# Performance work log

Hardware: AMD Instinct MI355X
Metric: run time of the kernel (lower is better)

The kernel has to match this reference:

```python
import jax, jax.numpy as jnp
import numpy as np

N_NODES = 50000
N_EDGES = 400000
NFEAT, NHID2, NHID3, NHID4, NCLASS = 500, 128, 128, 64, 40


def setup_inputs() -> dict:
    key = jax.random.key(0)
    ks = jax.random.split(key, 20)
    s = 0.05
    inp = {
        'x': jax.random.normal(ks[0], (N_NODES, NFEAT), jnp.float32),
        'src': jax.random.randint(ks[1], (4, N_EDGES), 0, N_NODES, jnp.int64 if jax.config.jax_enable_x64 else jnp.int32),
        'dst': jax.random.randint(ks[2], (4, N_EDGES), 0, N_NODES, jnp.int64 if jax.config.jax_enable_x64 else jnp.int32),
        'val': jax.random.uniform(ks[3], (4, N_EDGES), jnp.float32),
        'Wa': jax.random.normal(ks[4], (4, NFEAT, NHID2), jnp.float32) * s,
        'ba': jax.random.normal(ks[5], (4, NHID2), jnp.float32) * s,
        'Wb': jax.random.normal(ks[6], (4, NHID2, NHID3), jnp.float32) * s,
        'bb': jax.random.normal(ks[7], (4, NHID3), jnp.float32) * s,
        'Wc': jax.random.normal(ks[8], (4, NHID3, NHID4), jnp.float32) * s,
        'bc': jax.random.normal(ks[9], (4, NHID4), jnp.float32) * s,
        'dW': jax.random.normal(ks[10], (5, NHID4, NCLASS), jnp.float32) * s,
        'db': jax.random.normal(ks[11], (5, NCLASS), jnp.float32) * s,
        'e1W': jax.random.normal(ks[12], (4 * NHID4, NHID2), jnp.float32) * s,
        'e1b': jax.random.normal(ks[13], (NHID2,), jnp.float32) * s,
        'e2W': jax.random.normal(ks[14], (NHID2, NHID3), jnp.float32) * s,
        'e2b': jax.random.normal(ks[15], (NHID3,), jnp.float32) * s,
        'e3W': jax.random.normal(ks[16], (NHID3, NHID4), jnp.float32) * s,
        'e3b': jax.random.normal(ks[17], (NHID4,), jnp.float32) * s,
    }
    return inp


def _gcn(h, W, b, src, dst, val):
    # support = h @ W ; out = spmm(adj, support) + b  (Kipf GraphConvolution)
    support = h @ W                                   # [N, out]
    msg = support[src] * val[:, None]                 # [E, out] gather + scale
    return jax.ops.segment_sum(msg, dst, num_segments=N_NODES) + b


def reference(x, src, dst, val, Wa, ba, Wb, bb, Wc, bc, dW, db, e1W, e1b, e2W, e2b, e3W, e3b):
    # One GCN branch: relu(gcn) -> relu(gcn) -> gcn (dropout is inference no-op)
    def branch(Wa_i, ba_i, Wb_i, bb_i, Wc_i, bc_i, src_i, dst_i, val_i):
        h = jax.nn.relu(_gcn(x, Wa_i, ba_i, src_i, dst_i, val_i))
        h = jax.nn.relu(_gcn(h, Wb_i, bb_i, src_i, dst_i, val_i))
        return _gcn(h, Wc_i, bc_i, src_i, dst_i, val_i)  # pre-ReLU branch output

    xb = jax.vmap(branch)(Wa, ba, Wb, bb, Wc, bc, src, dst, val)  # [4, N, nhid4]

    # per-branch dense heads on relu(branch output)
    dense_out = jnp.einsum('knd,kdc->knc', jax.nn.relu(xb), dW[:4]) + db[:4, None, :]

    # ensemble MLP on concat(x1,x2,x3,x4)
    cat = jnp.transpose(xb, (1, 0, 2)).reshape(N_NODES, 4 * NHID4)
    e = jax.nn.relu(cat @ e1W + e1b)
    e = jax.nn.relu(e @ e2W + e2b)
    e = jax.nn.relu(e @ e3W + e3b)
    out5 = e @ dW[4] + db[4]

    return (dense_out[0], dense_out[1], dense_out[2], dense_out[3], out5)
```

## Files before the change

### kernel.cpp

```cpp
#include <hip/hip_runtime.h>
#include <stdint.h>

#define NN 50000
#define NE 400000
#define MPAD 50048
#define NF 500
#define KP 512
#define NBK 196

typedef __bf16 bf16;
typedef __bf16 bf16x8 __attribute__((ext_vector_type(8)));
typedef float  f32x4  __attribute__((ext_vector_type(4)));

__device__ __forceinline__ void gload16(const void* g, void* l) {
  __builtin_amdgcn_global_load_lds(
      (__attribute__((address_space(1))) void*)g,
      (__attribute__((address_space(3))) void*)l, 16, 0, 0);
}

__device__ __forceinline__ uint32_t packbf2(float a, float b) {
  union { bf16 h[2]; uint32_t u; } c;
  c.h[0] = (bf16)a; c.h[1] = (bf16)b;
  return c.u;
}

__global__ void k_conv_x(const float* __restrict__ x, bf16* __restrict__ xbf) {
  int idx = blockIdx.x * 256 + threadIdx.x;
  if (idx >= NN * KP) return;
  int n = idx >> 9, c = idx & (KP - 1);
  float v = (c < NF) ? x[n * NF + c] : 0.f;
  xbf[idx] = (bf16)v;
}

__global__ void k_conv_waT(const float* __restrict__ Wa, bf16* __restrict__ WaT) {
  int idx = blockIdx.x * 256 + threadIdx.x;
  if (idx >= 4 * 128 * KP) return;
  int b = idx >> 16;
  int r = idx & 65535;
  int n = r >> 9, k = r & 511;
  float v = (k < NF) ? Wa[(b * NF + k) * 128 + n] : 0.f;
  WaT[idx] = (bf16)v;
}

__global__ void k_conv_wT(const float* __restrict__ W, bf16* __restrict__ WT, int Kd, int Nd) {
  int idx = blockIdx.x * 256 + threadIdx.x;
  int tot = Kd * Nd;
  if (idx >= tot) return;
  int n = idx / Kd, k = idx - n * Kd;
  WT[(size_t)blockIdx.y * tot + idx] = (bf16)W[(size_t)blockIdx.y * tot + k * Nd + n];
}

__global__ void __launch_bounds__(256) k_bhist(const int* __restrict__ dst, int* __restrict__ bcnt) {
  __shared__ int h[256];
  int t = threadIdx.x;
  int z = blockIdx.z;
  h[t] = 0;
  __syncthreads();
  int e0 = blockIdx.x * 4096;
#pragma unroll
  for (int i = 0; i < 16; ++i) {
    int e = e0 + i * 256 + t;
    if (e < NE) atomicAdd(&h[dst[z * NE + e] >> 8], 1);
  }
  __syncthreads();
  if (t < NBK && h[t] > 0) atomicAdd(&bcnt[z * NBK + t], h[t]);
}

__global__ void __launch_bounds__(256) k_bscan(const int* __restrict__ bcnt,
                                               int* __restrict__ bases, int* __restrict__ gfill,
                                               int* __restrict__ offs) {
  __shared__ int ps[256];
  int t = threadIdx.x;
  for (int z = 0; z < 4; ++z) {
    int c = (t < NBK) ? bcnt[z * NBK + t] : 0;
    ps[t] = c;
    __syncthreads();
    for (int d = 1; d < 256; d <<= 1) {
      int v = (t >= d) ? ps[t - d] : 0;
      __syncthreads();
      ps[t] += v;
      __syncthreads();
    }
    if (t < NBK) {
      int ex = ps[t] - c;
      bases[z * (NBK + 1) + t] = ex;
      gfill[z * NBK + t] = ex;
      if (t == NBK - 1) bases[z * (NBK + 1) + NBK] = ps[t];
    }
    if (t == 0) offs[z * (NN + 1) + NN] = NE;
    __syncthreads();
  }
}

__global__ void __launch_bounds__(256) k_bin(const int* __restrict__ src, const int* __restrict__ dst,
                                             const float* __restrict__ val, int* __restrict__ gfill,
                                             int4* __restrict__ staging) {
  __shared__ int h[256];
  __shared__ int f2[256];
  __shared__ int base[256];
  int t = threadIdx.x;
  int z = blockIdx.z;
  h[t] = 0; f2[t] = 0;
  __syncthreads();
  int e0 = blockIdx.x * 4096;
  int se[16], sd[16], sv[16];
#pragma unroll
  for (int i = 0; i < 16; ++i) {
    int e = e0 + i * 256 + t;
    sd[i] = -1;
    if (e < NE) {
      sd[i] = dst[z * NE + e];
      se[i] = src[z * NE + e];
      sv[i] = ((const int*)val)[z * NE + e];
      atomicAdd(&h[sd[i] >> 8], 1);
    }
  }
  __syncthreads();
  if (t < NBK) {
    int c = h[t];
    base[t] = c ? atomicAdd(&gfill[z * NBK + t], c) : 0;
  }
  __syncthreads();
#pragma unroll
  for (int i = 0; i < 16; ++i) {
    if (sd[i] >= 0) {
      int bkt = sd[i] >> 8;
      int loc = atomicAdd(&f2[bkt], 1);
      staging[(size_t)z * NE + base[bkt] + loc] = make_int4(se[i], sd[i], sv[i], 0);
    }
  }
}

__global__ void __launch_bounds__(256) k_fine(const int4* __restrict__ staging,
                                              const int* __restrict__ bases,
                                              int* __restrict__ offs, int2* __restrict__ edata) {
  __shared__ int cnts[256];
  __shared__ int ps[256];
  __shared__ int exl[256];
  __shared__ int fl[256];
  int t = threadIdx.x;
  int z = blockIdx.z;
  int bkt = blockIdx.x;
  int base = bases[z * (NBK + 1) + bkt];
  int endp = bases[z * (NBK + 1) + bkt + 1];
  cnts[t] = 0; fl[t] = 0;
  __syncthreads();
  for (int e = base + t; e < endp; e += 256) {
    int dl = staging[(size_t)z * NE + e].y & 255;
    atomicAdd(&cnts[dl], 1);
  }
  __syncthreads();
  ps[t] = cnts[t];
  __syncthreads();
  for (int d = 1; d < 256; d <<= 1) {
    int v = (t >= d) ? ps[t - d] : 0;
    __syncthreads();
    ps[t] += v;
    __syncthreads();
  }
  exl[t] = ps[t] - cnts[t];
  int node0 = bkt * 256;
  if (node0 + t < NN) offs[z * (NN + 1) + node0 + t] = base + exl[t];
  __syncthreads();
  for (int e = base + t; e < endp; e += 256) {
    int4 g = staging[(size_t)z * NE + e];
    int dl = g.y & 255;
    int r = atomicAdd(&fl[dl], 1);
    edata[(size_t)z * NE + base + exl[dl] + r] = make_int2(g.x, g.z);
  }
}

template <int DIM>
__global__ void __launch_bounds__(256) k_spmm(
    const bf16* __restrict__ sup, const int* __restrict__ offs,
    const int2* __restrict__ edata,
    const float* __restrict__ bias, bf16* __restrict__ out,
    int ldOut, long long outBr, int relu) {
  constexpr int LPS = DIM / 8;
  constexpr int SLOTS = 64 / LPS;
  int b = blockIdx.z;
  int lane = threadIdx.x & 63;
  int slot = lane / LPS;
  int fl = lane % LPS;
  int n = blockIdx.x * 4 + (threadIdx.x >> 6);
  if (n >= NN) return;
  const int* o = offs + b * (NN + 1);
  int e0 = o[n], e1 = o[n + 1];
  const bf16* supb = sup + (size_t)b * MPAD * DIM;
  const int2* eb = edata + (size_t)b * NE;

  float a[8];
#pragma unroll
  for (int j = 0; j < 8; ++j) a[j] = 0.f;

  int e = e0 + slot;
  for (; e + SLOTS < e1; e += 2 * SLOTS) {
    int2 p0 = eb[e];
    int2 p1 = eb[e + SLOTS];
    float v0 = __int_as_float(p0.y);
    float v1 = __int_as_float(p1.y);
    bf16x8 r0 = *(const bf16x8*)(supb + (size_t)p0.x * DIM + fl * 8);
    bf16x8 r1 = *(const bf16x8*)(supb + (size_t)p1.x * DIM + fl * 8);
#pragma unroll
    for (int j = 0; j < 8; ++j) a[j] = fmaf(v0, (float)r0[j], a[j]);
#pragma unroll
    for (int j = 0; j < 8; ++j) a[j] = fmaf(v1, (float)r1[j], a[j]);
  }
  if (e < e1) {
    int2 p0 = eb[e];
    float v0 = __int_as_float(p0.y);
    bf16x8 r0 = *(const bf16x8*)(supb + (size_t)p0.x * DIM + fl * 8);
#pragma unroll
    for (int j = 0; j < 8; ++j) a[j] = fmaf(v0, (float)r0[j], a[j]);
  }

#pragma unroll
  for (int m = LPS; m < 64; m <<= 1) {
#pragma unroll
    for (int j = 0; j < 8; ++j) a[j] += __shfl_xor(a[j], m, 64);
  }

  if (slot == 0) {
    const float* bi = bias + b * DIM + fl * 8;
#pragma unroll
    for (int j = 0; j < 8; ++j) {
      a[j] += bi[j];
      if (relu) a[j] = fmaxf(a[j], 0.f);
    }
    union { bf16 h[8]; uint4 u4; } pk;
#pragma unroll
    for (int j = 0; j < 8; ++j) pk.h[j] = (bf16)a[j];
    *(uint4*)(out + (size_t)b * outBr + (size_t)n * ldOut + fl * 8) = pk.u4;
  }
}

template <int BN, bool BR>
__global__ void __launch_bounds__(256) k_gemm(
    const bf16* __restrict__ A, const bf16* __restrict__ B, bf16* __restrict__ C,
    const float* __restrict__ bias, int K, int ldA, int ldC,
    size_t sA, size_t sB, size_t sC) {
  constexpr int WN = BN / 2;
  constexpr int NFR = WN / 16;
  constexpr int BL = BN / 32;
  __shared__ __align__(16) unsigned char sa[128 * 128];
  __shared__ __align__(16) unsigned char sb[BN * 128];
  int tid = threadIdx.x;
  int lane = tid & 63;
  int wid = tid >> 6;
  int wm = wid & 1, wn = wid >> 1;
  const bf16* Ab = A + sA * blockIdx.z;
  const bf16* Bb = B + sB * blockIdx.z;
  bf16* Cb = C + sC * blockIdx.z;
  int gm0 = blockIdx.x * 128;

  f32x4 acc[4][NFR];
#pragma unroll
  for (int i = 0; i < 4; ++i)
#pragma unroll
    for (int j = 0; j < NFR; ++j) acc[i][j] = (f32x4){0.f, 0.f, 0.f, 0.f};

  for (int kt = 0; kt < K; kt += 64) {
#pragma unroll
    for (int i = 0; i < 4; ++i) {
      int lb = (wid * 4 + i) * 1024 + lane * 16;
      int r = lb >> 7;
      int c = (lb >> 4) & 7;
      gload16(Ab + (size_t)(gm0 + r) * ldA + kt + ((c ^ (r & 7)) << 3),
              &sa[(wid * 4 + i) * 1024]);
    }
#pragma unroll
    for (int i = 0; i < BL; ++i) {
      int lb = (wid * BL + i) * 1024 + lane * 16;
      int r = lb >> 7;
      int c = (lb >> 4) & 7;
      gload16(Bb + (size_t)r * K + kt + ((c ^ (r & 7)) << 3),
              &sb[(wid * BL + i) * 1024]);
    }
    __syncthreads();
#pragma unroll
    for (int kk = 0; kk < 2; ++kk) {
      bf16x8 ar[4], br[NFR];
#pragma unroll
      for (int mi = 0; mi < 4; ++mi) {
        int r = wm * 64 + mi * 16 + (lane & 15);
        int c = (kk * 4 + (lane >> 4)) ^ (r & 7);
        ar[mi] = *(const bf16x8*)&sa[r * 128 + c * 16];
      }
#pragma unroll
      for (int ni = 0; ni < NFR; ++ni) {
        int r = wn * WN + ni * 16 + (lane & 15);
        int c = (kk * 4 + (lane >> 4)) ^ (r & 7);
        br[ni] = *(const bf16x8*)&sb[r * 128 + c * 16];
      }
#pragma unroll
      for (int mi = 0; mi < 4; ++mi)
#pragma unroll
        for (int ni = 0; ni < NFR; ++ni)
          acc[mi][ni] = __builtin_amdgcn_mfma_f32_16x16x32_bf16(br[ni], ar[mi], acc[mi][ni], 0, 0, 0);
    }
    __syncthreads();
  }

#pragma unroll
  for (int mi = 0; mi < 4; ++mi) {
    int m = gm0 + wm * 64 + mi * 16 + (lane & 15);
#pragma unroll
    for (int ni = 0; ni < NFR; ++ni) {
      int n0 = wn * WN + ni * 16 + ((lane >> 4) << 2);
      f32x4 v = acc[mi][ni];
      if (BR) {
        const f32x4 bv = *(const f32x4*)&bias[n0];
        v[0] = fmaxf(v[0] + bv[0], 0.f);
        v[1] = fmaxf(v[1] + bv[1], 0.f);
        v[2] = fmaxf(v[2] + bv[2], 0.f);
        v[3] = fmaxf(v[3] + bv[3], 0.f);
      }
      uint2 st;
      st.x = packbf2(v[0], v[1]);
      st.y = packbf2(v[2], v[3]);
      *(uint2*)(Cb + (size_t)m * ldC + n0) = st;
    }
  }
}

__global__ void k_head(const bf16* __restrict__ X, int ldX,
                       const float* __restrict__ W, const float* __restrict__ bias,
                       float* __restrict__ out) {
  int idx = blockIdx.x * 256 + threadIdx.x;
  if (idx >= NN * 40) return;
  int n = idx / 40, c = idx - n * 40;
  const bf16* xr = X + (size_t)n * ldX;
  float acc = bias[c];
#pragma unroll
  for (int d2 = 0; d2 < 32; ++d2) {
    union { uint32_t u; bf16 h[2]; } cv;
    cv.u = *(const uint32_t*)(xr + d2 * 2);
    acc = fmaf(fmaxf((float)cv.h[0], 0.f), W[(d2 * 2) * 40 + c], acc);
    acc = fmaf(fmaxf((float)cv.h[1], 0.f), W[(d2 * 2 + 1) * 40 + c], acc);
  }
  out[idx] = acc;
}

extern "C" void kernel_launch(void* const* d_in, const int* in_sizes, int n_in,
                              void* d_out, int out_size, void* d_ws, size_t ws_size,
                              hipStream_t stream) {
  (void)in_sizes; (void)n_in; (void)out_size; (void)ws_size;
  const float* x   = (const float*)d_in[0];
  const int*   src = (const int*)d_in[1];
  const int*   dst = (const int*)d_in[2];
  const float* val = (const float*)d_in[3];
  const float* Wa  = (const float*)d_in[4];
  const float* ba  = (const float*)d_in[5];
  const float* Wb  = (const float*)d_in[6];
  const float* bb  = (const float*)d_in[7];
  const float* Wc  = (const float*)d_in[8];
  const float* bc  = (const float*)d_in[9];
  const float* dW  = (const float*)d_in[10];
  const float* db  = (const float*)d_in[11];
  const float* e1W = (const float*)d_in[12];
  const float* e1b = (const float*)d_in[13];
  const float* e2W = (const float*)d_in[14];
  const float* e2b = (const float*)d_in[15];
  const float* e3W = (const float*)d_in[16];
  const float* e3b = (const float*)d_in[17];
  float* out = (float*)d_out;

  uint8_t* ws = (uint8_t*)d_ws;
  size_t off = 0;
  auto carve = [&](size_t sz) -> void* {
    void* p = ws + off;
    off = (off + sz + 255) & ~(size_t)255;
    return p;
  };

  bf16* xbf   = (bf16*)carve((size_t)MPAD * KP * 2);
  bf16* WaT   = (bf16*)carve((size_t)4 * 128 * KP * 2);
  bf16* WbT   = (bf16*)carve((size_t)4 * 128 * 128 * 2);
  bf16* WcT   = (bf16*)carve((size_t)4 * 64 * 128 * 2);
  bf16* e1WT  = (bf16*)carve((size_t)128 * 256 * 2);
  bf16* e2WT  = (bf16*)carve((size_t)128 * 128 * 2);
  bf16* e3WT  = (bf16*)carve((size_t)64 * 128 * 2);
  bf16* bufS  = (bf16*)carve((size_t)4 * MPAD * 128 * 2);
  bf16* bufH  = (bf16*)carve((size_t)4 * MPAD * 128 * 2);
  int*  bcnt  = (int*)carve((size_t)4 * NBK * 4);
  int*  gfill = (int*)carve((size_t)4 * NBK * 4);
  int*  bases = (int*)carve((size_t)4 * (NBK + 1) * 4);
  int*  offs  = (int*)carve((size_t)4 * (NN + 1) * 4);
  int2* edata = (int2*)carve((size_t)4 * NE * 8);
  int4* staging = (int4*)bufS;
  bf16* e1buf = xbf;
  bf16* e2buf = xbf + (size_t)MPAD * 128;
  bf16* e3buf = xbf + (size_t)2 * MPAD * 128;

  hipMemsetAsync(bcnt, 0, (size_t)4 * NBK * 4, stream);

  k_conv_x  <<<(NN * KP + 255) / 256, 256, 0, stream>>>(x, xbf);
  k_conv_waT<<<(4 * 128 * KP + 255) / 256, 256, 0, stream>>>(Wa, WaT);
  k_conv_wT <<<dim3((128 * 128 + 255) / 256, 4), 256, 0, stream>>>(Wb, WbT, 128, 128);
  k_conv_wT <<<dim3((128 * 64 + 255) / 256, 4), 256, 0, stream>>>(Wc, WcT, 128, 64);
  k_conv_wT <<<dim3((256 * 128 + 255) / 256, 1), 256, 0, stream>>>(e1W, e1WT, 256, 128);
  k_conv_wT <<<dim3((128 * 128 + 255) / 256, 1), 256, 0, stream>>>(e2W, e2WT, 128, 128);
  k_conv_wT <<<dim3((128 * 64 + 255) / 256, 1), 256, 0, stream>>>(e3W, e3WT, 128, 64);

  const int EB = (NE + 4095) / 4096;
  k_bhist<<<dim3(EB, 1, 4), 256, 0, stream>>>(dst, bcnt);
  k_bscan<<<1, 256, 0, stream>>>(bcnt, bases, gfill, offs);
  k_bin  <<<dim3(EB, 1, 4), 256, 0, stream>>>(src, dst, val, gfill, staging);
  k_fine <<<dim3(NBK, 1, 4), 256, 0, stream>>>(staging, bases, offs, edata);

  const dim3 gemmGrid4(MPAD / 128, 1, 4);
  const dim3 gemmGrid1(MPAD / 128, 1, 1);

  k_gemm<128, false><<<gemmGrid4, 256, 0, stream>>>(xbf, WaT, bufS, nullptr, KP, KP, 128,
                                                    0, (size_t)128 * KP, (size_t)MPAD * 128);
  k_spmm<128><<<dim3((NN + 3) / 4, 1, 4), 256, 0, stream>>>(bufS, offs, edata, ba, bufH,
                                                            128, (long long)MPAD * 128, 1);
  k_gemm<128, false><<<gemmGrid4, 256, 0, stream>>>(bufH, WbT, bufS, nullptr, 128, 128, 128,
                                                    (size_t)MPAD * 128, (size_t)128 * 128, (size_t)MPAD * 128);
  k_spmm<128><<<dim3((NN + 3) / 4, 1, 4), 256, 0, stream>>>(bufS, offs, edata, bb, bufH,
                                                            128, (long long)MPAD * 128, 1);
  k_gemm<64, false><<<gemmGrid4, 256, 0, stream>>>(bufH, WcT, bufS, nullptr, 128, 128, 64,
                                                   (size_t)MPAD * 128, (size_t)64 * 128, (size_t)MPAD * 64);
  k_spmm<64><<<dim3((NN + 3) / 4, 1, 4), 256, 0, stream>>>(bufS, offs, edata, bc, bufH,
                                                           256, 64, 0);
  for (int k = 0; k < 4; ++k)
    k_head<<<(NN * 40 + 255) / 256, 256, 0, stream>>>(bufH + k * 64, 256,
                                                      dW + (size_t)k * 64 * 40, db + k * 40,
                                                      out + (size_t)k * NN * 40);
  k_gemm<128, true><<<gemmGrid1, 256, 0, stream>>>(bufH, e1WT, e1buf, e1b, 256, 256, 128, 0, 0, 0);
  k_gemm<128, true><<<gemmGrid1, 256, 0, stream>>>(e1buf, e2WT, e2buf, e2b, 128, 128, 128, 0, 0, 0);
  k_gemm<64,  true><<<gemmGrid1, 256, 0, stream>>>(e2buf, e3WT, e3buf, e3b, 128, 128, 64, 0, 0, 0);
  k_head<<<(NN * 40 + 255) / 256, 256, 0, stream>>>(e3buf, 64, dW + (size_t)4 * 64 * 40, db + 4 * 40,
                                                    out + (size_t)4 * NN * 40);
}
```

Before: 776.1 us.

## Fix SpMM lane mapping to 8 slots and interleave branches across blocks

The SpMM kernel now always uses 8 edge slots per wavefront, with each lane covering DIM/64 chunks of 8 features, instead of slot counts that depend on DIM. This gives more edges in flight for the 128-wide layers and more independent loads per lane. The grid is flattened to 1D and remapped so that consecutive blocks alternate across the four branches in pairs, which may spread gather traffic across the different branch buffers. The cost is more accumulator registers per lane and more strided row reads per edge.

```diff
diff --git a/kernel.cpp b/kernel.cpp
--- a/kernel.cpp
+++ b/kernel.cpp
@@ -176,61 +176,81 @@
     const int2* __restrict__ edata,
     const float* __restrict__ bias, bf16* __restrict__ out,
     int ldOut, long long outBr, int relu) {
-  constexpr int LPS = DIM / 8;
-  constexpr int SLOTS = 64 / LPS;
-  int b = blockIdx.z;
+  constexpr int SLOTS = 8;
+  constexpr int LOADS = DIM / 64;
+  constexpr int NA = LOADS * 8;
   int lane = threadIdx.x & 63;
-  int slot = lane / LPS;
-  int fl = lane % LPS;
-  int n = blockIdx.x * 4 + (threadIdx.x >> 6);
+  int slot = lane >> 3;
+  int fl = lane & 7;
+  int lin = blockIdx.x;
+  int x8 = lin & 7;
+  int b = x8 >> 1;
+  int cnt = (lin >> 3) * 2 + (x8 & 1);
+  int n = cnt * 4 + (threadIdx.x >> 6);
   if (n >= NN) return;
   const int* o = offs + b * (NN + 1);
   int e0 = o[n], e1 = o[n + 1];
   const bf16* supb = sup + (size_t)b * MPAD * DIM;
   const int2* eb = edata + (size_t)b * NE;
 
-  float a[8];
-#pragma unroll
-  for (int j = 0; j < 8; ++j) a[j] = 0.f;
+  float a[NA];
+#pragma unroll
+  for (int j = 0; j < NA; ++j) a[j] = 0.f;
 
   int e = e0 + slot;
   for (; e + SLOTS < e1; e += 2 * SLOTS) {
     int2 p0 = eb[e];
     int2 p1 = eb[e + SLOTS];
+    const bf16* r0p = supb + (size_t)p0.x * DIM + fl * 8;
+    const bf16* r1p = supb + (size_t)p1.x * DIM + fl * 8;
+    bf16x8 r0[LOADS], r1[LOADS];
+#pragma unroll
+    for (int l = 0; l < LOADS; ++l) {
+      r0[l] = *(const bf16x8*)(r0p + l * 64);
+      r1[l] = *(const bf16x8*)(r1p + l * 64);
+    }
     float v0 = __int_as_float(p0.y);
     float v1 = __int_as_float(p1.y);
-    bf16x8 r0 = *(const bf16x8*)(supb + (size_t)p0.x * DIM + fl * 8);
-    bf16x8 r1 = *(const bf16x8*)(supb + (size_t)p1.x * DIM + fl * 8);
-#pragma unroll
-    for (int j = 0; j < 8; ++j) a[j] = fmaf(v0, (float)r0[j], a[j]);
-#pragma unroll
-    for (int j = 0; j < 8; ++j) a[j] = fmaf(v1, (float)r1[j], a[j]);
+#pragma unroll
+    for (int l = 0; l < LOADS; ++l)
+#pragma unroll
+      for (int j = 0; j < 8; ++j) {
+        a[l * 8 + j] = fmaf(v0, (float)r0[l][j], a[l * 8 + j]);
+        a[l * 8 + j] = fmaf(v1, (float)r1[l][j], a[l * 8 + j]);
+      }
   }
   if (e < e1) {
     int2 p0 = eb[e];
+    const bf16* r0p = supb + (size_t)p0.x * DIM + fl * 8;
+    bf16x8 r0[LOADS];
+#pragma unroll
+    for (int l = 0; l < LOADS; ++l) r0[l] = *(const bf16x8*)(r0p + l * 64);
     float v0 = __int_as_float(p0.y);
-    bf16x8 r0 = *(const bf16x8*)(supb + (size_t)p0.x * DIM + fl * 8);
-#pragma unroll
-    for (int j = 0; j < 8; ++j) a[j] = fmaf(v0, (float)r0[j], a[j]);
-  }
-
-#pragma unroll
-  for (int m = LPS; m < 64; m <<= 1) {
-#pragma unroll
-    for (int j = 0; j < 8; ++j) a[j] += __shfl_xor(a[j], m, 64);
+#pragma unroll
+    for (int l = 0; l < LOADS; ++l)
+#pragma unroll
+      for (int j = 0; j < 8; ++j) a[l * 8 + j] = fmaf(v0, (float)r0[l][j], a[l * 8 + j]);
+  }
+
+#pragma unroll
+  for (int m = 8; m < 64; m <<= 1) {
+#pragma unroll
+    for (int j = 0; j < NA; ++j) a[j] += __shfl_xor(a[j], m, 64);
   }
 
   if (slot == 0) {
-    const float* bi = bias + b * DIM + fl * 8;
-#pragma unroll
-    for (int j = 0; j < 8; ++j) {
-      a[j] += bi[j];
-      if (relu) a[j] = fmaxf(a[j], 0.f);
-    }
-    union { bf16 h[8]; uint4 u4; } pk;
-#pragma unroll
-    for (int j = 0; j < 8; ++j) pk.h[j] = (bf16)a[j];
-    *(uint4*)(out + (size_t)b * outBr + (size_t)n * ldOut + fl * 8) = pk.u4;
+#pragma unroll
+    for (int l = 0; l < LOADS; ++l) {
+      const float* bi = bias + b * DIM + l * 64 + fl * 8;
+      union { bf16 h[8]; uint4 u4; } pk;
+#pragma unroll
+      for (int j = 0; j < 8; ++j) {
+        float v = a[l * 8 + j] + bi[j];
+        if (relu) v = fmaxf(v, 0.f);
+        pk.h[j] = (bf16)v;
+      }
+      *(uint4*)(out + (size_t)b * outBr + (size_t)n * ldOut + l * 64 + fl * 8) = pk.u4;
+    }
   }
 }
 
@@ -410,19 +430,20 @@
 
   const dim3 gemmGrid4(MPAD / 128, 1, 4);
   const dim3 gemmGrid1(MPAD / 128, 1, 1);
+  const int spmmGrid = 4 * ((NN + 3) / 4);
 
   k_gemm<128, false><<<gemmGrid4, 256, 0, stream>>>(xbf, WaT, bufS, nullptr, KP, KP, 128,
                                                     0, (size_t)128 * KP, (size_t)MPAD * 128);
-  k_spmm<128><<<dim3((NN + 3) / 4, 1, 4), 256, 0, stream>>>(bufS, offs, edata, ba, bufH,
-                                                            128, (long long)MPAD * 128, 1);
+  k_spmm<128><<<spmmGrid, 256, 0, stream>>>(bufS, offs, edata, ba, bufH,
+                                            128, (long long)MPAD * 128, 1);
   k_gemm<128, false><<<gemmGrid4, 256, 0, stream>>>(bufH, WbT, bufS, nullptr, 128, 128, 128,
                                                     (size_t)MPAD * 128, (size_t)128 * 128, (size_t)MPAD * 128);
-  k_spmm<128><<<dim3((NN + 3) / 4, 1, 4), 256, 0, stream>>>(bufS, offs, edata, bb, bufH,
-                                                            128, (long long)MPAD * 128, 1);
+  k_spmm<128><<<spmmGrid, 256, 0, stream>>>(bufS, offs, edata, bb, bufH,
+                                            128, (long long)MPAD * 128, 1);
   k_gemm<64, false><<<gemmGrid4, 256, 0, stream>>>(bufH, WcT, bufS, nullptr, 128, 128, 64,
                                                    (size_t)MPAD * 128, (size_t)64 * 128, (size_t)MPAD * 64);
-  k_spmm<64><<<dim3((NN + 3) / 4, 1, 4), 256, 0, stream>>>(bufS, offs, edata, bc, bufH,
-                                                           256, 64, 0);
+  k_spmm<64><<<spmmGrid, 256, 0, stream>>>(bufS, offs, edata, bc, bufH,
+                                           256, 64, 0);
   for (int k = 0; k < 4; ++k)
     k_head<<<(NN * 40 + 255) / 256, 256, 0, stream>>>(bufH + k * 64, 256,
                                                       dW + (size_t)k * 64 * 40, db + k * 40,
```

New measurement: 819.1 us. 1.06x slower.
